# Optimization experiments

Measured on AMD Instinct MI355X. Metric: run time of the kernel, lower is better.

The kernel has to match this reference:

```python
import jax, jax.numpy as jnp
import numpy as np

EPS = 1e-8  # torch F.cosine_similarity denominator clamp

def _row_cosine(a, b):
    # cosine similarity along last dim, rowwise: (N, D), (N, D) -> (N,)
    dot = jnp.sum(a * b, axis=-1)
    na = jnp.linalg.norm(a, axis=-1)
    nb = jnp.linalg.norm(b, axis=-1)
    return dot / jnp.maximum(na * nb, EPS)

def setup_inputs() -> dict:
    key = jax.random.key(0)
    k0, k1, k2, k3 = jax.random.split(key, 4)
    B, D, N = 4096, 256, 262144
    return {
        "anchor_emb": jax.random.normal(k0, (B, D), dtype=jnp.float32),
        "pos_emb": jax.random.normal(k1, (B, D), dtype=jnp.float32),
        "neg_emb": jax.random.normal(k2, (N, D), dtype=jnp.float32),
        "neg_batch_indices": jax.random.randint(k3, (N,), 0, B, dtype=jnp.int64),
    }

def reference(anchor_emb, pos_emb, neg_emb, neg_batch_indices):
    margin = 0.5
    B = anchor_emb.shape[0]
    # (B,) positive similarities
    pos_sim = _row_cosine(anchor_emb, pos_emb)
    # gather each negative's anchor: (N, D)
    anchor_g = anchor_emb[neg_batch_indices]
    neg_sims = _row_cosine(anchor_g, neg_emb)              # (N,)
    triplet = jnp.maximum(margin + neg_sims - pos_sim[neg_batch_indices], 0.0)  # (N,)
    # segment mean per batch item; empty segments contribute 0
    sums = jax.ops.segment_sum(triplet, neg_batch_indices, num_segments=B)
    counts = jax.ops.segment_sum(jnp.ones_like(triplet), neg_batch_indices, num_segments=B)
    means = jnp.where(counts > 0, sums / jnp.maximum(counts, 1.0), 0.0)
    return jnp.sum(means) / B
```

## Files before the change

kernel.cpp:

```cpp
#include <hip/hip_runtime.h>
#include <math.h>

#define EPS 1e-8f
#define MARGIN 0.5f
#define NEG_PER_WAVE 32

typedef float   f4 __attribute__((ext_vector_type(4)));
typedef _Float16 h4 __attribute__((ext_vector_type(4)));

__device__ __forceinline__ float dot4(const f4 a, const f4 b) {
    return a.x * b.x + a.y * b.y + a.z * b.z + a.w * b.w;
}
__device__ __forceinline__ float dot4h(const h4 a, const f4 b) {
    return (float)a.x * b.x + (float)a.y * b.y + (float)a.z * b.z + (float)a.w * b.w;
}


__global__ void pos_h_kernel(const float* __restrict__ anchor,
                             const float* __restrict__ pos,
                             _Float16* __restrict__ a_h,
                             float* __restrict__ ps,
                             float* __restrict__ sums,
                             float* __restrict__ counts,
                             int B) {
    const int tid  = blockIdx.x * blockDim.x + threadIdx.x;
    const int row  = tid >> 6;
    const int lane = threadIdx.x & 63;

    if (tid < B) sums[tid] = 0.0f;
    else if (tid < 2 * B) counts[tid - B] = 0.0f;

    if (row >= B) return;

    const f4 a = *(reinterpret_cast<const f4*>(anchor + (size_t)row * 256) + lane);
    const f4 p = *(reinterpret_cast<const f4*>(pos    + (size_t)row * 256) + lane);

    float dot = dot4(a, p);
    float na  = dot4(a, a);
    float nb  = dot4(p, p);

    #pragma unroll
    for (int off = 32; off > 0; off >>= 1) {
        dot += __shfl_xor(dot, off);
        na  += __shfl_xor(na,  off);
        nb  += __shfl_xor(nb,  off);
    }
    const float sna   = sqrtf(na);
    const float scale = 1.0f / fmaxf(sna, 1e-20f);

    h4 ah;
    ah.x = (_Float16)(a.x * scale);
    ah.y = (_Float16)(a.y * scale);
    ah.z = (_Float16)(a.z * scale);
    ah.w = (_Float16)(a.w * scale);
    *(reinterpret_cast<h4*>(a_h + (size_t)row * 256) + lane) = ah;

    if (lane == 0)
        ps[row] = dot / fmaxf(sna * sqrtf(nb), EPS);
}

__global__ void __launch_bounds__(256) neg_h_kernel(
        const _Float16* __restrict__ a_h,
        const float* __restrict__ neg,
        const int*  __restrict__ idx,
        const float* __restrict__ ps,
        float* __restrict__ sums,
        float* __restrict__ counts,
        int N) {
    const int lane  = threadIdx.x & 63;
    const int wid   = threadIdx.x >> 6;
    const int group = lane >> 4;
    const int glane = lane & 15;
    const long long base =
        ((long long)blockIdx.x * (blockDim.x >> 6) + wid) * NEG_PER_WAVE;
    if (base >= N) return;

    if (base + NEG_PER_WAVE <= N) {
        #pragma unroll 2
        for (int it = 0; it < NEG_PER_WAVE; it += 4) {
            const long long n = base + it + group;
            const int b = idx[n];

            const f4* nr = reinterpret_cast<const f4*>(neg + (size_t)n * 256);
            const h4* ar = reinterpret_cast<const h4*>(a_h + (size_t)b * 256);

            const f4 v0 = __builtin_nontemporal_load(nr +  0 + glane);
            const f4 v1 = __builtin_nontemporal_load(nr + 16 + glane);
            const f4 v2 = __builtin_nontemporal_load(nr + 32 + glane);
            const f4 v3 = __builtin_nontemporal_load(nr + 48 + glane);
            const h4 a0 = ar[ 0 + glane], a1 = ar[16 + glane],
                     a2 = ar[32 + glane], a3 = ar[48 + glane];

            float d = dot4h(a0, v0) + dot4h(a1, v1) + dot4h(a2, v2) + dot4h(a3, v3);
            float q = dot4(v0, v0) + dot4(v1, v1) + dot4(v2, v2) + dot4(v3, v3);

            #pragma unroll
            for (int off = 8; off > 0; off >>= 1) {
                d += __shfl_xor(d, off);
                q += __shfl_xor(q, off);
            }
            if (glane == 0) {
                float t = fmaxf(MARGIN + d / sqrtf(fmaxf(q, 1e-30f)) - ps[b], 0.0f);
                atomicAdd(&sums[b], t);
                atomicAdd(&counts[b], 1.0f);
            }
        }
    } else {
        for (int it = 0; it < NEG_PER_WAVE; it += 4) {
            const long long n = base + it + group;
            if (n >= N) continue;
            const int b = idx[n];
            const f4* nr = reinterpret_cast<const f4*>(neg + (size_t)n * 256);
            const h4* ar = reinterpret_cast<const h4*>(a_h + (size_t)b * 256);
            const f4 v0 = __builtin_nontemporal_load(nr +  0 + glane);
            const f4 v1 = __builtin_nontemporal_load(nr + 16 + glane);
            const f4 v2 = __builtin_nontemporal_load(nr + 32 + glane);
            const f4 v3 = __builtin_nontemporal_load(nr + 48 + glane);
            const h4 a0 = ar[ 0 + glane], a1 = ar[16 + glane],
                     a2 = ar[32 + glane], a3 = ar[48 + glane];
            float d = dot4h(a0, v0) + dot4h(a1, v1) + dot4h(a2, v2) + dot4h(a3, v3);
            float q = dot4(v0, v0) + dot4(v1, v1) + dot4(v2, v2) + dot4(v3, v3);
            #pragma unroll
            for (int off = 8; off > 0; off >>= 1) {
                d += __shfl_xor(d, off);
                q += __shfl_xor(q, off);
            }
            if (glane == 0) {
                float t = fmaxf(MARGIN + d / sqrtf(fmaxf(q, 1e-30f)) - ps[b], 0.0f);
                atomicAdd(&sums[b], t);
                atomicAdd(&counts[b], 1.0f);
            }
        }
    }
}


__global__ void pos_sim_kernel(const float* __restrict__ anchor,
                               const float* __restrict__ pos,
                               float2* __restrict__ pn,
                               float* __restrict__ sums,
                               float* __restrict__ counts,
                               int B) {
    const int tid  = blockIdx.x * blockDim.x + threadIdx.x;
    const int wave = tid >> 6;
    const int lane = threadIdx.x & 63;
    if (tid < B) sums[tid] = 0.0f;
    else if (tid < 2 * B) counts[tid - B] = 0.0f;
    if (wave >= B) return;
    const f4 a = *(reinterpret_cast<const f4*>(anchor + (size_t)wave * 256) + lane);
    const f4 p = *(reinterpret_cast<const f4*>(pos    + (size_t)wave * 256) + lane);
    float dot = dot4(a, p), na = dot4(a, a), nb = dot4(p, p);
    #pragma unroll
    for (int off = 32; off > 0; off >>= 1) {
        dot += __shfl_xor(dot, off);
        na  += __shfl_xor(na,  off);
        nb  += __shfl_xor(nb,  off);
    }
    if (lane == 0) {
        float sna = sqrtf(na);
        float2 r; r.x = dot / fmaxf(sna * sqrtf(nb), EPS); r.y = sna;
        pn[wave] = r;
    }
}

__global__ void __launch_bounds__(256) neg_kernel(
        const float* __restrict__ anchor,
        const float* __restrict__ neg,
        const int*  __restrict__ idx,
        const float2* __restrict__ pn,
        float* __restrict__ sums,
        float* __restrict__ counts,
        int N) {
    const int lane  = threadIdx.x & 63;
    const int wid   = threadIdx.x >> 6;
    const int group = lane >> 4;
    const int glane = lane & 15;
    const long long base =
        ((long long)blockIdx.x * (blockDim.x >> 6) + wid) * NEG_PER_WAVE;
    if (base >= N) return;
    for (int it = 0; it < NEG_PER_WAVE; it += 4) {
        const long long n = base + it + group;
        if (n >= N) continue;
        const int b = idx[n];
        const f4* ar = reinterpret_cast<const f4*>(anchor + (size_t)b * 256);
        const f4* nr = reinterpret_cast<const f4*>(neg + (size_t)n * 256);
        float d = 0.0f, q = 0.0f;
        #pragma unroll
        for (int c = 0; c < 4; ++c) {
            const f4 a = ar[c * 16 + glane];
            const f4 v = __builtin_nontemporal_load(nr + c * 16 + glane);
            d += dot4(a, v); q += dot4(v, v);
        }
        #pragma unroll
        for (int off = 8; off > 0; off >>= 1) {
            d += __shfl_xor(d, off);
            q += __shfl_xor(q, off);
        }
        if (glane == 0) {
            const float2 p = pn[b];
            float t = fmaxf(MARGIN + d / fmaxf(p.y * sqrtf(q), EPS) - p.x, 0.0f);
            atomicAdd(&sums[b], t);
            atomicAdd(&counts[b], 1.0f);
        }
    }
}

__global__ void __launch_bounds__(1024) finalize_kernel(
        const float* __restrict__ sums,
        const float* __restrict__ counts,
        float* __restrict__ out, int B) {
    float local = 0.0f;
    for (int i = threadIdx.x; i < B; i += blockDim.x) {
        float c = counts[i];
        local += (c > 0.0f) ? (sums[i] / c) : 0.0f;
    }
    #pragma unroll
    for (int off = 32; off > 0; off >>= 1)
        local += __shfl_xor(local, off);

    __shared__ float ws[16];
    const int wid = threadIdx.x >> 6;
    if ((threadIdx.x & 63) == 0) ws[wid] = local;
    __syncthreads();
    if (threadIdx.x == 0) {
        float tot = 0.0f;
        const int nw = blockDim.x >> 6;
        for (int w = 0; w < nw; ++w) tot += ws[w];
        out[0] = tot / (float)B;
    }
}

extern "C" void kernel_launch(void* const* d_in, const int* in_sizes, int n_in,
                              void* d_out, int out_size, void* d_ws, size_t ws_size,
                              hipStream_t stream) {
    const float* anchor = (const float*)d_in[0];
    const float* pos    = (const float*)d_in[1];
    const float* neg    = (const float*)d_in[2];
    const int*   idx    = (const int*)d_in[3];

    const int D = 256;
    int B = in_sizes[0] / D;
    int N = in_sizes[3];

    const size_t need_h = (size_t)B * 256 * sizeof(_Float16)
                        + (size_t)B * 3 * sizeof(float);

    const int threads = 256;
    const int negs_per_block = (threads / 64) * NEG_PER_WAVE;
    const int nblocks = (N + negs_per_block - 1) / negs_per_block;

    if (ws_size >= need_h) {
        _Float16* a_h   = (_Float16*)d_ws;
        float*    ps    = (float*)(a_h + (size_t)B * 256);
        float*    sums  = ps + B;
        float*    counts = sums + B;

        pos_h_kernel<<<(B + 3) / 4, threads, 0, stream>>>(anchor, pos, a_h, ps,
                                                          sums, counts, B);
        neg_h_kernel<<<nblocks, threads, 0, stream>>>(a_h, neg, idx, ps,
                                                      sums, counts, N);
        finalize_kernel<<<1, 1024, 0, stream>>>(sums, counts, (float*)d_out, B);
    } else {
        float2* pn     = (float2*)d_ws;
        float*  sums   = (float*)(pn + B);
        float*  counts = sums + B;

        pos_sim_kernel<<<(B + 3) / 4, threads, 0, stream>>>(anchor, pos, pn,
                                                            sums, counts, B);
        neg_kernel<<<nblocks, threads, 0, stream>>>(anchor, neg, idx, pn,
                                                    sums, counts, N);
        finalize_kernel<<<1, 1024, 0, stream>>>(sums, counts, (float*)d_out, B);
    }
}
```

Measured before the change: 68.94 us.

## Pack sum and count into one 64-bit fixed-point atomic per negative

```diff
diff --git a/kernel.cpp b/kernel.cpp
--- a/kernel.cpp
+++ b/kernel.cpp
@@ -4,8 +4,10 @@
 #define EPS 1e-8f
 #define MARGIN 0.5f
 #define NEG_PER_WAVE 32
-
-typedef float   f4 __attribute__((ext_vector_type(4)));
+#define FIXSCALE 1048576.0f
+#define MASK40 ((1ULL << 40) - 1)
+
+typedef float    f4 __attribute__((ext_vector_type(4)));
 typedef _Float16 h4 __attribute__((ext_vector_type(4)));
 
 __device__ __forceinline__ float dot4(const f4 a, const f4 b) {
@@ -20,15 +22,13 @@
                              const float* __restrict__ pos,
                              _Float16* __restrict__ a_h,
                              float* __restrict__ ps,
-                             float* __restrict__ sums,
-                             float* __restrict__ counts,
+                             unsigned long long* __restrict__ acc,
                              int B) {
     const int tid  = blockIdx.x * blockDim.x + threadIdx.x;
     const int row  = tid >> 6;
     const int lane = threadIdx.x & 63;
 
-    if (tid < B) sums[tid] = 0.0f;
-    else if (tid < 2 * B) counts[tid - B] = 0.0f;
+    if (tid < 2 * B) ((unsigned int*)acc)[tid] = 0u;
 
     if (row >= B) return;
 
@@ -64,24 +64,29 @@
         const float* __restrict__ neg,
         const int*  __restrict__ idx,
         const float* __restrict__ ps,
-        float* __restrict__ sums,
-        float* __restrict__ counts,
+        unsigned long long* __restrict__ acc,
         int N) {
+    __shared__ int   sb[4][NEG_PER_WAVE];
+    __shared__ float ssim[4][NEG_PER_WAVE];
+
     const int lane  = threadIdx.x & 63;
     const int wid   = threadIdx.x >> 6;
     const int group = lane >> 4;
     const int glane = lane & 15;
     const long long base =
         ((long long)blockIdx.x * (blockDim.x >> 6) + wid) * NEG_PER_WAVE;
-    if (base >= N) return;
-
-    if (base + NEG_PER_WAVE <= N) {
+
+    if (lane < NEG_PER_WAVE) sb[wid][lane] = -1;
+
+    if (base < N) {
         #pragma unroll 2
         for (int it = 0; it < NEG_PER_WAVE; it += 4) {
             const long long n = base + it + group;
-            const int b = idx[n];
-
-            const f4* nr = reinterpret_cast<const f4*>(neg + (size_t)n * 256);
+            const bool valid = (n < N);
+            const long long ns = valid ? n : (long long)0;
+            const int b = valid ? idx[ns] : 0;
+
+            const f4* nr = reinterpret_cast<const f4*>(neg + (size_t)ns * 256);
             const h4* ar = reinterpret_cast<const h4*>(a_h + (size_t)b * 256);
 
             const f4 v0 = __builtin_nontemporal_load(nr +  0 + glane);
@@ -99,38 +104,50 @@
                 d += __shfl_xor(d, off);
                 q += __shfl_xor(q, off);
             }
-            if (glane == 0) {
-                float t = fmaxf(MARGIN + d / sqrtf(fmaxf(q, 1e-30f)) - ps[b], 0.0f);
-                atomicAdd(&sums[b], t);
-                atomicAdd(&counts[b], 1.0f);
+            if (glane == 0 && valid) {
+                sb[wid][it + group]   = b;
+                ssim[wid][it + group] = d * rsqrtf(fmaxf(q, 1e-30f));
             }
         }
-    } else {
-        for (int it = 0; it < NEG_PER_WAVE; it += 4) {
-            const long long n = base + it + group;
-            if (n >= N) continue;
-            const int b = idx[n];
-            const f4* nr = reinterpret_cast<const f4*>(neg + (size_t)n * 256);
-            const h4* ar = reinterpret_cast<const h4*>(a_h + (size_t)b * 256);
-            const f4 v0 = __builtin_nontemporal_load(nr +  0 + glane);
-            const f4 v1 = __builtin_nontemporal_load(nr + 16 + glane);
-            const f4 v2 = __builtin_nontemporal_load(nr + 32 + glane);
-            const f4 v3 = __builtin_nontemporal_load(nr + 48 + glane);
-            const h4 a0 = ar[ 0 + glane], a1 = ar[16 + glane],
-                     a2 = ar[32 + glane], a3 = ar[48 + glane];
-            float d = dot4h(a0, v0) + dot4h(a1, v1) + dot4h(a2, v2) + dot4h(a3, v3);
-            float q = dot4(v0, v0) + dot4(v1, v1) + dot4(v2, v2) + dot4(v3, v3);
-            #pragma unroll
-            for (int off = 8; off > 0; off >>= 1) {
-                d += __shfl_xor(d, off);
-                q += __shfl_xor(q, off);
-            }
-            if (glane == 0) {
-                float t = fmaxf(MARGIN + d / sqrtf(fmaxf(q, 1e-30f)) - ps[b], 0.0f);
-                atomicAdd(&sums[b], t);
-                atomicAdd(&counts[b], 1.0f);
-            }
-        }
+    }
+
+    __syncthreads();
+
+    if (lane < NEG_PER_WAVE) {
+        const int b = sb[wid][lane];
+        if (b >= 0) {
+            const float sim = ssim[wid][lane];
+            const float t = fmaxf(MARGIN + sim - ps[b], 0.0f);
+            const unsigned long long pk =
+                (unsigned long long)(t * FIXSCALE + 0.5f) + (1ULL << 40);
+            atomicAdd(&acc[b], pk);
+        }
+    }
+}
+
+__global__ void __launch_bounds__(1024) finalize_packed_kernel(
+        const unsigned long long* __restrict__ acc,
+        float* __restrict__ out, int B) {
+    float local = 0.0f;
+    for (int i = threadIdx.x; i < B; i += blockDim.x) {
+        const unsigned long long v = acc[i];
+        const float c = (float)(v >> 40);
+        const float s = (float)(v & MASK40) * (1.0f / FIXSCALE);
+        local += (c > 0.0f) ? (s / c) : 0.0f;
+    }
+    #pragma unroll
+    for (int off = 32; off > 0; off >>= 1)
+        local += __shfl_xor(local, off);
+
+    __shared__ float ws[16];
+    const int wid = threadIdx.x >> 6;
+    if ((threadIdx.x & 63) == 0) ws[wid] = local;
+    __syncthreads();
+    if (threadIdx.x == 0) {
+        float tot = 0.0f;
+        const int nw = blockDim.x >> 6;
+        for (int w = 0; w < nw; ++w) tot += ws[w];
+        out[0] = tot / (float)B;
     }
 }
 
@@ -243,23 +260,23 @@
     int N = in_sizes[3];
 
     const size_t need_h = (size_t)B * 256 * sizeof(_Float16)
-                        + (size_t)B * 3 * sizeof(float);
+                        + (size_t)B * sizeof(float)
+                        + (size_t)B * sizeof(unsigned long long);
 
     const int threads = 256;
     const int negs_per_block = (threads / 64) * NEG_PER_WAVE;
     const int nblocks = (N + negs_per_block - 1) / negs_per_block;
 
     if (ws_size >= need_h) {
-        _Float16* a_h   = (_Float16*)d_ws;
-        float*    ps    = (float*)(a_h + (size_t)B * 256);
-        float*    sums  = ps + B;
-        float*    counts = sums + B;
+        _Float16*           a_h = (_Float16*)d_ws;
+        float*              ps  = (float*)(a_h + (size_t)B * 256);
+        unsigned long long* acc = (unsigned long long*)(ps + B);
 
         pos_h_kernel<<<(B + 3) / 4, threads, 0, stream>>>(anchor, pos, a_h, ps,
-                                                          sums, counts, B);
+                                                          acc, B);
         neg_h_kernel<<<nblocks, threads, 0, stream>>>(a_h, neg, idx, ps,
-                                                      sums, counts, N);
-        finalize_kernel<<<1, 1024, 0, stream>>>(sums, counts, (float*)d_out, B);
+                                                      acc, N);
+        finalize_packed_kernel<<<1, 1024, 0, stream>>>(acc, (float*)d_out, B);
     } else {
         float2* pn     = (float2*)d_ws;
         float*  sums   = (float*)(pn + B);
```

New measurement: 63.41 us. -8.0%, faster.
